# Optimization experiments

Hardware: AMD Instinct MI355X
Metric: run time of the kernel (lower is better)

## Reference

```python
import jax, jax.numpy as jnp
import numpy as np

VOCAB, VDIM, DDIM, BATCH = 50257, 300, 512, 16


def setup_inputs() -> dict:
    key = jax.random.key(0)
    k1, k2, k3, k4, k5 = jax.random.split(key, 5)
    return {
        "decoder_hidden": jax.random.normal(k1, (BATCH, DDIM), dtype=jnp.float32),
        "embedding_vocab": jax.random.normal(k2, (VOCAB, VDIM), dtype=jnp.float32),
        "W_dec": jax.random.normal(k3, (VDIM, DDIM), dtype=jnp.float32) * (1.0 / np.sqrt(DDIM)),
        "b_dec": jax.random.normal(k4, (VDIM,), dtype=jnp.float32) * 0.01,
        "W_full": jax.random.normal(k5, (VDIM,), dtype=jnp.float32) * (1.0 / np.sqrt(VDIM)),
        "b_full": jnp.zeros((), dtype=jnp.float32),
    }


def reference(decoder_hidden, embedding_vocab, W_dec, b_dec, W_full, b_full):
    # query: (B, vocab_dim) = decoder_att(decoder_hidden)
    query = decoder_hidden @ W_dec.T + b_dec
    # additive scores: relu(vocab + query) projected to scalar -> (B, V)
    hidden = jax.nn.relu(embedding_vocab[None, :, :] + query[:, None, :])  # (B, V, D)
    att = jnp.einsum("bvd,d->bv", hidden, W_full) + b_full
    alpha = jax.nn.softmax(att, axis=1)  # softmax over vocab
    # weighted sum of vocab embeddings: (B, vocab_dim)
    attention_weighted_encoding = jnp.einsum("bv,vd->bd", alpha, embedding_vocab)
    return attention_weighted_encoding, alpha
```

## Files before the change

kernel.cpp:

```cpp
#include <hip/hip_runtime.h>

constexpr int V  = 50257;
constexpr int D  = 300;
constexpr int KD = 512;
constexpr int B  = 16;

constexpr int ROWS = 32;
constexpr int NB_ATT = (V + ROWS - 1) / ROWS;
constexpr int NC  = 512;
constexpr int RPC = (V + NC - 1) / NC;

constexpr float NEG_HUGE = -1.0e30f;

constexpr size_t WS_QT   = 0;
constexpr size_t WS_STAT = 4800;
constexpr size_t WS_MS   = WS_STAT + (size_t)NB_ATT * 32;
constexpr size_t WS_PART = WS_MS + 32;
constexpr size_t WS_TMP  = WS_PART + (size_t)NC * 4800;

struct f4 { float v[4]; };
__device__ __forceinline__ f4 ld4(const float* p) {
    float4 t = *(const float4*)p;
    return {t.x, t.y, t.z, t.w};
}

__global__ void __launch_bounds__(256) k_query(
    const float* __restrict__ dh, const float* __restrict__ Wdec,
    const float* __restrict__ bdec, float* __restrict__ q_t)
{
    int wid  = (blockIdx.x * 256 + threadIdx.x) >> 6;
    int lane = threadIdx.x & 63;
    if (wid >= D * B) return;
    int d = wid >> 4, b = wid & 15;
    const float* wrow = Wdec + (size_t)d * KD;
    const float* hrow = dh + (size_t)b * KD;
    float s = 0.f;
    for (int k = lane; k < KD; k += 64) s += wrow[k] * hrow[k];
    #pragma unroll
    for (int off = 32; off; off >>= 1) s += __shfl_down(s, off, 64);
    if (lane == 0) q_t[d * 16 + b] = s + bdec[d];
}

__global__ void __launch_bounds__(256) k_att(
    const float* __restrict__ E, const float* __restrict__ q_t,
    const float* __restrict__ wf, const float* __restrict__ bf,
    float* __restrict__ att, float* __restrict__ blkstats)
{
    __shared__ float sq[4864];
    __shared__ float sw[304];
    int t = threadIdx.x;
    for (int i4 = t * 4; i4 < 4800; i4 += 1024) {
        float4 qv = *(const float4*)(q_t + i4);
        int d = i4 >> 4, bq = (i4 & 15) >> 2;
        int col = (bq + (d >> 2)) & 3;
        *(float4*)(sq + (d << 4) + (col << 2)) = qv;
    }
    if (t < 64) sq[4800 + t] = 0.f;
    for (int i = t; i < 304; i += 256) sw[i] = (i < 300) ? wf[i] : 0.f;
    __syncthreads();

    const int bg   = t >> 6;
    const int lane = t & 63;
    const int rs   = lane >> 2;
    const int p    = lane & 3;
    const int p4   = p << 2;
    const int rot4 = ((bg + p) & 3) << 2;
    const int v0   = blockIdx.x << 5;

    const float* ep[2];
    bool rvalid[2];
    #pragma unroll
    for (int j = 0; j < 2; ++j) {
        int row = v0 + rs + (j << 4);
        rvalid[j] = row < V;
        ep[j] = E + (size_t)(rvalid[j] ? row : (V - 1)) * D;
    }

    float acc[2][4];
    #pragma unroll
    for (int j = 0; j < 2; ++j)
        #pragma unroll
        for (int b = 0; b < 4; ++b) acc[j][b] = 0.f;

    f4 ec[2], en[2];
    #pragma unroll
    for (int j = 0; j < 2; ++j) ec[j] = ld4(ep[j] + p4);

    #pragma unroll 2
    for (int k = 0; k < 19; ++k) {
        int d0 = (k << 4) + p4;
        int dn = d0 + 16;
        int dns = (dn < D) ? dn : 0;
        #pragma unroll
        for (int j = 0; j < 2; ++j) en[j] = ld4(ep[j] + dns);

        f4 wv = ld4(sw + d0);
        #pragma unroll
        for (int i = 0; i < 4; ++i) {
            f4 qv = ld4(sq + ((d0 + i) << 4) + rot4);
            float wi = wv.v[i];
            #pragma unroll
            for (int j = 0; j < 2; ++j) {
                float e = ec[j].v[i];
                #pragma unroll
                for (int b = 0; b < 4; ++b)
                    acc[j][b] = fmaf(fmaxf(e + qv.v[b], 0.f), wi, acc[j][b]);
            }
        }
        #pragma unroll
        for (int j = 0; j < 2; ++j) ec[j] = en[j];
    }

    #pragma unroll
    for (int j = 0; j < 2; ++j)
        #pragma unroll
        for (int b = 0; b < 4; ++b) {
            float s = acc[j][b];
            s += __shfl_xor(s, 1, 64);
            s += __shfl_xor(s, 2, 64);
            acc[j][b] = s;
        }

    float bfull = bf[0];
    float vj[2];
    float m_l = NEG_HUGE;
    #pragma unroll
    for (int j = 0; j < 2; ++j) {
        float s = (p == 0) ? acc[j][0] : (p == 1) ? acc[j][1]
                : (p == 2) ? acc[j][2] : acc[j][3];
        s += bfull;
        int row = v0 + rs + (j << 4);
        if (rvalid[j]) att[(size_t)((bg << 2) + p) * V + row] = s;
        vj[j] = rvalid[j] ? s : NEG_HUGE;
        m_l = fmaxf(m_l, vj[j]);
    }
    float s_l = __expf(vj[0] - m_l) + __expf(vj[1] - m_l);

    #pragma unroll
    for (int sh = 2; sh < 6; ++sh) {
        int mask = 1 << sh;
        float mo = __shfl_xor(m_l, mask, 64);
        float so = __shfl_xor(s_l, mask, 64);
        float mn = fmaxf(m_l, mo);
        s_l = s_l * __expf(m_l - mn) + so * __expf(mo - mn);
        m_l = mn;
    }
    if (rs == 0) {
        size_t idx = ((size_t)blockIdx.x * 16 + (bg << 2) + p) * 2;
        blkstats[idx]     = m_l;
        blkstats[idx + 1] = s_l;
    }
}

__global__ void __launch_bounds__(64) k_combine(
    const float* __restrict__ blkstats, float* __restrict__ MS)
{
    int b = blockIdx.x, lane = threadIdx.x;
    float m = NEG_HUGE;
    for (int c = lane; c < NB_ATT; c += 64)
        m = fmaxf(m, blkstats[(size_t)(c * 16 + b) * 2]);
    #pragma unroll
    for (int off = 32; off; off >>= 1) m = fmaxf(m, __shfl_xor(m, off, 64));
    float s = 0.f;
    for (int c = lane; c < NB_ATT; c += 64)
        s += blkstats[(size_t)(c * 16 + b) * 2 + 1] *
             __expf(blkstats[(size_t)(c * 16 + b) * 2] - m);
    #pragma unroll
    for (int off = 32; off; off >>= 1) s += __shfl_xor(s, off, 64);
    if (lane == 0) { MS[b * 2] = m; MS[b * 2 + 1] = 1.f / s; }
}

__global__ void __launch_bounds__(320) k_awsum(
    const float* __restrict__ E, float* __restrict__ att,
    const float* __restrict__ MS, float* __restrict__ partials)
{
    __shared__ float sal[RPC * 16];
    int c = blockIdx.x, t = threadIdx.x;
    int v0 = c * RPC;
    int n = V - v0;
    if (n > RPC) n = RPC;
    if (n < 0) n = 0;

    for (int i = t; i < RPC * 16; i += 320) {
        int b = i / RPC, vv = i - b * RPC;
        float a = 0.f;
        if (vv < n) {
            float M = MS[b * 2], invS = MS[b * 2 + 1];
            size_t gi = (size_t)b * V + v0 + vv;
            a = __expf(att[gi] - M) * invS;
            att[gi] = a;
        }
        sal[vv * 16 + b] = a;
    }
    __syncthreads();

    if (t < D) {
        float acc[16];
        #pragma unroll
        for (int b = 0; b < 16; ++b) acc[b] = 0.f;
        #pragma unroll 4
        for (int vv = 0; vv < n; ++vv) {
            float e = E[(size_t)(v0 + vv) * D + t];
            const float* ap = sal + vv * 16;
            f4 a0 = ld4(ap), a1 = ld4(ap + 4), a2 = ld4(ap + 8), a3 = ld4(ap + 12);
            #pragma unroll
            for (int b = 0; b < 4; ++b) {
                acc[b]      = fmaf(a0.v[b], e, acc[b]);
                acc[b + 4]  = fmaf(a1.v[b], e, acc[b + 4]);
                acc[b + 8]  = fmaf(a2.v[b], e, acc[b + 8]);
                acc[b + 12] = fmaf(a3.v[b], e, acc[b + 12]);
            }
        }
        #pragma unroll
        for (int b = 0; b < 16; ++b)
            partials[(size_t)c * 4800 + b * D + t] = acc[b];
    }
}

__global__ void __launch_bounds__(256) k_red1(
    const float* __restrict__ partials, float* __restrict__ tmp)
{
    int o4 = blockIdx.x * 256 + threadIdx.x;
    if (o4 >= 1200) return;
    int y = blockIdx.y;
    float4 s = {0.f, 0.f, 0.f, 0.f};
    for (int c = y * 32; c < y * 32 + 32; ++c) {
        float4 p = *(const float4*)(partials + (size_t)c * 4800 + o4 * 4);
        s.x += p.x; s.y += p.y; s.z += p.z; s.w += p.w;
    }
    *(float4*)(tmp + (size_t)y * 4800 + o4 * 4) = s;
}

__global__ void __launch_bounds__(256) k_red2(
    const float* __restrict__ tmp, float* __restrict__ out)
{
    int o4 = blockIdx.x * 256 + threadIdx.x;
    if (o4 >= 1200) return;
    float4 s = {0.f, 0.f, 0.f, 0.f};
    #pragma unroll
    for (int y = 0; y < 16; ++y) {
        float4 p = *(const float4*)(tmp + (size_t)y * 4800 + o4 * 4);
        s.x += p.x; s.y += p.y; s.z += p.z; s.w += p.w;
    }
    *(float4*)(out + o4 * 4) = s;
}

extern "C" void kernel_launch(void* const* d_in, const int* in_sizes, int n_in,
                              void* d_out, int out_size, void* d_ws, size_t ws_size,
                              hipStream_t stream) {
    const float* dh   = (const float*)d_in[0];
    const float* E    = (const float*)d_in[1];
    const float* Wdec = (const float*)d_in[2];
    const float* bdec = (const float*)d_in[3];
    const float* wf   = (const float*)d_in[4];
    const float* bf   = (const float*)d_in[5];
    float* out = (float*)d_out;
    float* ws  = (float*)d_ws;

    float* q_t   = ws + WS_QT;
    float* stats = ws + WS_STAT;
    float* MS    = ws + WS_MS;
    float* part  = ws + WS_PART;
    float* tmp   = ws + WS_TMP;
    float* att   = out + 4800;

    k_query<<<(D * B + 3) / 4, 256, 0, stream>>>(dh, Wdec, bdec, q_t);
    k_att<<<NB_ATT, 256, 0, stream>>>(E, q_t, wf, bf, att, stats);
    k_combine<<<B, 64, 0, stream>>>(stats, MS);
    k_awsum<<<NC, 320, 0, stream>>>(E, att, MS, part);
    k_red1<<<dim3(5, 16), 256, 0, stream>>>(part, tmp);
    k_red2<<<5, 256, 0, stream>>>(tmp, out);
}
```

Before: 73.43 us.

## Restructure attention-score kernel with LDS triple-buffered async loads and 64-row blocks

The score kernel now handles 64 vocab rows per block, with each thread computing all 16 batch entries for two rows over an 8-lane slice of the embedding dimension. Embedding tiles are streamed into LDS with global_load_lds in a three-stage buffer, waited on with explicit vmcnt and barriers, so loads overlap compute. Per-block softmax statistics are merged across waves in shared memory before being written out. The cost is more registers (32 accumulators), more LDS, half as many blocks, and a hand-written wait/barrier schedule that is fragile.

```diff
diff --git a/kernel.cpp b/kernel.cpp
--- a/kernel.cpp
+++ b/kernel.cpp
@@ -5,8 +5,9 @@
 constexpr int KD = 512;
 constexpr int B  = 16;
 
-constexpr int ROWS = 32;
+constexpr int ROWS = 64;
 constexpr int NB_ATT = (V + ROWS - 1) / ROWS;
+constexpr int NT = 10;
 constexpr int NC  = 512;
 constexpr int RPC = (V + NC - 1) / NC;
 
@@ -23,6 +24,9 @@
     float4 t = *(const float4*)p;
     return {t.x, t.y, t.z, t.w};
 }
+
+#define AS1 __attribute__((address_space(1)))
+#define AS3 __attribute__((address_space(3)))
 
 __global__ void __launch_bounds__(256) k_query(
     const float* __restrict__ dh, const float* __restrict__ Wdec,
@@ -46,110 +50,143 @@
     const float* __restrict__ wf, const float* __restrict__ bf,
     float* __restrict__ att, float* __restrict__ blkstats)
 {
-    __shared__ float sq[4864];
-    __shared__ float sw[304];
-    int t = threadIdx.x;
-    for (int i4 = t * 4; i4 < 4800; i4 += 1024) {
-        float4 qv = *(const float4*)(q_t + i4);
+    __shared__ float se[3 * 2048];
+    __shared__ float sq[5120];
+    __shared__ float sw[320];
+    __shared__ float smsM[64], smsS[64];
+
+    const int t = threadIdx.x;
+
+    for (int i4 = t * 4; i4 < 5120; i4 += 1024) {
+        float4 qv = make_float4(0.f, 0.f, 0.f, 0.f);
+        if (i4 < 4800) qv = *(const float4*)(q_t + i4);
         int d = i4 >> 4, bq = (i4 & 15) >> 2;
         int col = (bq + (d >> 2)) & 3;
         *(float4*)(sq + (d << 4) + (col << 2)) = qv;
     }
-    if (t < 64) sq[4800 + t] = 0.f;
-    for (int i = t; i < 304; i += 256) sw[i] = (i < 300) ? wf[i] : 0.f;
+    for (int i = t; i < 320; i += 256) sw[i] = (i < D) ? wf[i] : 0.f;
     __syncthreads();
 
-    const int bg   = t >> 6;
-    const int lane = t & 63;
-    const int rs   = lane >> 2;
-    const int p    = lane & 3;
-    const int p4   = p << 2;
-    const int rot4 = ((bg + p) & 3) << 2;
-    const int v0   = blockIdx.x << 5;
-
-    const float* ep[2];
-    bool rvalid[2];
-    #pragma unroll
-    for (int j = 0; j < 2; ++j) {
-        int row = v0 + rs + (j << 4);
-        rvalid[j] = row < V;
-        ep[j] = E + (size_t)(rvalid[j] ? row : (V - 1)) * D;
-    }
-
-    float acc[2][4];
-    #pragma unroll
-    for (int j = 0; j < 2; ++j)
+    const int v0   = blockIdx.x * ROWS;
+    const int slot = t & 7;
+    const int s4   = slot << 2;
+    const int rloc = t >> 3;
+    const int r0   = v0 + rloc;
+    const int r1   = r0 + 32;
+    const bool va0 = r0 < V, va1 = r1 < V;
+    const float* src0 = E + (size_t)(va0 ? r0 : (V - 1)) * D;
+    const float* src1 = E + (size_t)(va1 ? r1 : (V - 1)) * D;
+
+    float acc0[16], acc1[16];
+    #pragma unroll
+    for (int b = 0; b < 16; ++b) { acc0[b] = 0.f; acc1[b] = 0.f; }
+
+#define STAGE(TT, BI) do {                                                    \
+    int dd = (TT) * 32 + s4;                                                  \
+    if (dd >= D) dd = 0;                                                      \
+    float* lb = se + (BI) * 2048 + (t << 2);                                  \
+    __builtin_amdgcn_global_load_lds((const AS1 void*)(src0 + dd),            \
+                                     (AS3 void*)lb, 16, 0, 0);                \
+    __builtin_amdgcn_global_load_lds((const AS1 void*)(src1 + dd),            \
+                                     (AS3 void*)(lb + 1024), 16, 0, 0);       \
+} while (0)
+
+#define COMPUTE(TT, BI) do {                                                  \
+    const float* buf = se + (BI) * 2048;                                      \
+    f4 e0 = ld4(buf + (t << 2));                                              \
+    f4 e1 = ld4(buf + (t << 2) + 1024);                                       \
+    int dbase = (TT) * 32 + s4;                                               \
+    _Pragma("unroll")                                                         \
+    for (int i = 0; i < 4; ++i) {                                             \
+        int d = dbase + i;                                                    \
+        float wi = sw[d];                                                     \
+        const float* qrow = sq + (d << 4);                                    \
+        int rr = d >> 2;                                                      \
+        _Pragma("unroll")                                                     \
+        for (int bq = 0; bq < 4; ++bq) {                                      \
+            f4 qv = ld4(qrow + (((bq + rr) & 3) << 2));                       \
+            _Pragma("unroll")                                                 \
+            for (int bl = 0; bl < 4; ++bl) {                                  \
+                acc0[bq * 4 + bl] = fmaf(fmaxf(e0.v[i] + qv.v[bl], 0.f), wi,  \
+                                         acc0[bq * 4 + bl]);                  \
+                acc1[bq * 4 + bl] = fmaf(fmaxf(e1.v[i] + qv.v[bl], 0.f), wi,  \
+                                         acc1[bq * 4 + bl]);                  \
+            }                                                                 \
+        }                                                                     \
+    }                                                                         \
+} while (0)
+
+    STAGE(0, 0);
+    STAGE(1, 1);
+    for (int tt = 0; tt < NT - 1; ++tt) {
+        asm volatile("s_waitcnt vmcnt(2)" ::: "memory");
+        __builtin_amdgcn_s_barrier();
+        __builtin_amdgcn_sched_barrier(0);
+        if (tt < NT - 2) STAGE(tt + 2, (tt + 2) % 3);
+        COMPUTE(tt, tt % 3);
+    }
+    asm volatile("s_waitcnt vmcnt(0)" ::: "memory");
+    __builtin_amdgcn_s_barrier();
+    __builtin_amdgcn_sched_barrier(0);
+    COMPUTE(NT - 1, (NT - 1) % 3);
+
+    #pragma unroll
+    for (int b = 0; b < 16; ++b) {
+        float x0 = acc0[b], x1 = acc1[b];
+        x0 += __shfl_xor(x0, 1, 64); x1 += __shfl_xor(x1, 1, 64);
+        x0 += __shfl_xor(x0, 2, 64); x1 += __shfl_xor(x1, 2, 64);
+        x0 += __shfl_xor(x0, 4, 64); x1 += __shfl_xor(x1, 4, 64);
+        acc0[b] = x0; acc1[b] = x1;
+    }
+
+    float bfull = bf[0];
+    int b0 = slot * 2;
+    float v00 = acc0[b0]     + bfull;
+    float v01 = acc0[b0 + 1] + bfull;
+    float v10 = acc1[b0]     + bfull;
+    float v11 = acc1[b0 + 1] + bfull;
+    if (va0) {
+        att[(size_t)b0 * V + r0]       = v00;
+        att[(size_t)(b0 + 1) * V + r0] = v01;
+    }
+    if (va1) {
+        att[(size_t)b0 * V + r1]       = v10;
+        att[(size_t)(b0 + 1) * V + r1] = v11;
+    }
+    float m0 = fmaxf(va0 ? v00 : NEG_HUGE, va1 ? v10 : NEG_HUGE);
+    float m1 = fmaxf(va0 ? v01 : NEG_HUGE, va1 ? v11 : NEG_HUGE);
+    float s0 = (va0 ? __expf(v00 - m0) : 0.f) + (va1 ? __expf(v10 - m0) : 0.f);
+    float s1 = (va0 ? __expf(v01 - m1) : 0.f) + (va1 ? __expf(v11 - m1) : 0.f);
+
+    #pragma unroll
+    for (int mask = 8; mask <= 32; mask <<= 1) {
+        float mo = __shfl_xor(m0, mask, 64), so = __shfl_xor(s0, mask, 64);
+        float mn = fmaxf(m0, mo);
+        s0 = s0 * __expf(m0 - mn) + so * __expf(mo - mn); m0 = mn;
+        mo = __shfl_xor(m1, mask, 64); so = __shfl_xor(s1, mask, 64);
+        mn = fmaxf(m1, mo);
+        s1 = s1 * __expf(m1 - mn) + so * __expf(mo - mn); m1 = mn;
+    }
+    int wv = t >> 6;
+    if ((t & 63) < 8) {
+        smsM[wv * 16 + b0] = m0;     smsS[wv * 16 + b0] = s0;
+        smsM[wv * 16 + b0 + 1] = m1; smsS[wv * 16 + b0 + 1] = s1;
+    }
+    __syncthreads();
+    if (t < 16) {
+        float m = smsM[t], s = smsS[t];
         #pragma unroll
-        for (int b = 0; b < 4; ++b) acc[j][b] = 0.f;
-
-    f4 ec[2], en[2];
-    #pragma unroll
-    for (int j = 0; j < 2; ++j) ec[j] = ld4(ep[j] + p4);
-
-    #pragma unroll 2
-    for (int k = 0; k < 19; ++k) {
-        int d0 = (k << 4) + p4;
-        int dn = d0 + 16;
-        int dns = (dn < D) ? dn : 0;
-        #pragma unroll
-        for (int j = 0; j < 2; ++j) en[j] = ld4(ep[j] + dns);
-
-        f4 wv = ld4(sw + d0);
-        #pragma unroll
-        for (int i = 0; i < 4; ++i) {
-            f4 qv = ld4(sq + ((d0 + i) << 4) + rot4);
-            float wi = wv.v[i];
-            #pragma unroll
-            for (int j = 0; j < 2; ++j) {
-                float e = ec[j].v[i];
-                #pragma unroll
-                for (int b = 0; b < 4; ++b)
-                    acc[j][b] = fmaf(fmaxf(e + qv.v[b], 0.f), wi, acc[j][b]);
-            }
+        for (int w = 1; w < 4; ++w) {
+            float mo = smsM[w * 16 + t], so = smsS[w * 16 + t];
+            float mn = fmaxf(m, mo);
+            s = s * __expf(m - mn) + so * __expf(mo - mn);
+            m = mn;
         }
-        #pragma unroll
-        for (int j = 0; j < 2; ++j) ec[j] = en[j];
-    }
-
-    #pragma unroll
-    for (int j = 0; j < 2; ++j)
-        #pragma unroll
-        for (int b = 0; b < 4; ++b) {
-            float s = acc[j][b];
-            s += __shfl_xor(s, 1, 64);
-            s += __shfl_xor(s, 2, 64);
-            acc[j][b] = s;
-        }
-
-    float bfull = bf[0];
-    float vj[2];
-    float m_l = NEG_HUGE;
-    #pragma unroll
-    for (int j = 0; j < 2; ++j) {
-        float s = (p == 0) ? acc[j][0] : (p == 1) ? acc[j][1]
-                : (p == 2) ? acc[j][2] : acc[j][3];
-        s += bfull;
-        int row = v0 + rs + (j << 4);
-        if (rvalid[j]) att[(size_t)((bg << 2) + p) * V + row] = s;
-        vj[j] = rvalid[j] ? s : NEG_HUGE;
-        m_l = fmaxf(m_l, vj[j]);
-    }
-    float s_l = __expf(vj[0] - m_l) + __expf(vj[1] - m_l);
-
-    #pragma unroll
-    for (int sh = 2; sh < 6; ++sh) {
-        int mask = 1 << sh;
-        float mo = __shfl_xor(m_l, mask, 64);
-        float so = __shfl_xor(s_l, mask, 64);
-        float mn = fmaxf(m_l, mo);
-        s_l = s_l * __expf(m_l - mn) + so * __expf(mo - mn);
-        m_l = mn;
-    }
-    if (rs == 0) {
-        size_t idx = ((size_t)blockIdx.x * 16 + (bg << 2) + p) * 2;
-        blkstats[idx]     = m_l;
-        blkstats[idx + 1] = s_l;
-    }
+        blkstats[((size_t)blockIdx.x * 16 + t) * 2]     = m;
+        blkstats[((size_t)blockIdx.x * 16 + t) * 2 + 1] = s;
+    }
+#undef STAGE
+#undef COMPUTE
 }
 
 __global__ void __launch_bounds__(64) k_combine(
```

New measurement: 82.24 us. +12.0%, slower.
